# Kernel tuning notes

Measured on AMD Instinct MI355X. Metric: run time of the kernel, lower is better.

Reference implementation:

```python
import jax, jax.numpy as jnp
import jax.lax as lax
import numpy as np

# ---- Parallel3DGeometry constants ----
B, C = 1, 1
D, H, W = 64, 96, 96          # internal volume layout (z, y, x)
V, U, A = 64, 96, 90          # detector rows, detector cols, projection angles
SX = SY = SD = 1.0            # voxel size (x, y, z)
SU = SV = 1.0                 # detector spacing
NSTEPS = H + W + 2            # upper bound on voxels crossed by an XY ray
DIAG = float(np.sqrt(SX * SX + SY * SY))
EPS = 1e-12


def _t_for(p0, dp, pmin, pmax):
    # slab entry/exit parameters, matching torch _t_for (incl. parallel-ray cases)
    par = jnp.abs(dp) < EPS
    safe = jnp.where(par, 1.0, dp)
    t0 = (pmin - p0) / safe
    t1 = (pmax - p0) / safe
    lo = jnp.minimum(t0, t1)
    hi = jnp.maximum(t0, t1)
    inside = (p0 >= pmin) & (p0 <= pmax)
    lo = jnp.where(par, jnp.where(inside, -jnp.inf, jnp.inf), lo)
    hi = jnp.where(par, jnp.where(inside, jnp.inf, -jnp.inf), hi)
    return lo, hi


def _trace():
    """Vectorized Siddon XY traversal for all A*U rays.

    Returns Is, Js (int32 [A,U,NSTEPS]) voxel indices and Ws (f32 [A,U,NSTEPS])
    segment lengths (0 where the ray has exited / padded steps).
    """
    angles = jnp.linspace(0.0, np.pi, A, endpoint=False).astype(jnp.float32)
    cos_t = jnp.cos(angles)
    sin_t = jnp.sin(angles)
    u = (jnp.arange(U, dtype=jnp.float32) - (U - 1) / 2.0) * SU
    dx = jnp.broadcast_to(cos_t[:, None], (A, U)).reshape(-1)
    dy = jnp.broadcast_to(sin_t[:, None], (A, U)).reshape(-1)
    x0 = (-u[None, :] * sin_t[:, None]).reshape(-1)
    y0 = (u[None, :] * cos_t[:, None]).reshape(-1)

    x_min = -((W - 1) / 2.0) * SX; x_max = ((W - 1) / 2.0) * SX
    y_min = -((H - 1) / 2.0) * SY; y_max = ((H - 1) / 2.0) * SY
    tx0, tx1 = _t_for(x0, dx, x_min, x_max)
    ty0, ty1 = _t_for(y0, dy, y_min, y_max)
    t_entry = jnp.maximum(tx0, ty0)
    t_exit = jnp.minimum(tx1, ty1)
    alive0 = t_entry < t_exit
    te = jnp.where(alive0, t_entry, 0.0)
    tex = jnp.where(alive0, t_exit, 0.0)
    xe = x0 + te * dx
    ye = y0 + te * dy
    i0 = jnp.clip(jnp.round(xe / SX + (W - 1) / 2.0), 0, W - 1).astype(jnp.int32)
    j0 = jnp.clip(jnp.round(ye / SY + (H - 1) / 2.0), 0, H - 1).astype(jnp.int32)
    cxw = (W - 1) / 2.0 * SX
    cyh = (H - 1) / 2.0 * SY

    def body(st, _):
        i, j, x, y, t, alive = st
        valid = alive & (t < tex - EPS)
        fi = i.astype(jnp.float32)
        fj = j.astype(jnp.float32)
        xn = jnp.where(dx > 0, (fi + 0.5) * SX - cxw,
                       jnp.where(dx < 0, (fi - 0.5) * SX - cxw, jnp.inf))
        yn = jnp.where(dy > 0, (fj + 0.5) * SY - cyh,
                       jnp.where(dy < 0, (fj - 0.5) * SY - cyh, jnp.inf))
        okx = jnp.abs(dx) > EPS
        oky = jnp.abs(dy) > EPS
        tx = jnp.where(okx, (xn - x) / jnp.where(okx, dx, 1.0), jnp.inf)
        ty = jnp.where(oky, (yn - y) / jnp.where(oky, dy, 1.0), jnp.inf)
        dt = jnp.minimum(jnp.minimum(tx, ty), tex - t)
        seg = jnp.maximum(0.0, dt * DIAG / jnp.maximum(jnp.abs(dx) + jnp.abs(dy), EPS))
        w = jnp.where(valid, seg, 0.0)
        i_n = i + jnp.where(tx <= ty, jnp.where(dx > 0, 1, -1), 0)
        j_n = j + jnp.where(ty <= tx, jnp.where(dy > 0, 1, -1), 0)
        inb = (i_n >= 0) & (i_n < W) & (j_n >= 0) & (j_n < H)
        dts = jnp.where(valid, dt, 0.0)
        st2 = (jnp.where(valid, i_n, i), jnp.where(valid, j_n, j),
               x + dx * dts, y + dy * dts, t + dts, valid & inb)
        return st2, (i, j, w)

    init = (i0, j0, xe, ye, te, alive0)
    _, (Is, Js, Ws) = lax.scan(body, init, None, length=NSTEPS)
    # [NSTEPS, R] -> [A, U, NSTEPS]
    Is = Is.T.reshape(A, U, NSTEPS)
    Js = Js.T.reshape(A, U, NSTEPS)
    Ws = Ws.T.reshape(A, U, NSTEPS)
    return Is, Js, Ws


def _forward(vol):
    # model-facing [B,C,X,Y,Z] -> internal [B,C,D,H,W]
    vol_int = jnp.transpose(vol, (0, 1, 4, 3, 2))
    Is, Js, Ws = _trace()
    v_phys = (jnp.arange(V, dtype=jnp.float32) - (V - 1) / 2.0) * SV
    k = jnp.clip(jnp.round(v_phys / SD + (D - 1) / 2.0), 0, D - 1).astype(jnp.int32)
    # gather voxel values along every ray: [B,C,V,A,U,NSTEPS]
    g = vol_int[:, :, k[:, None, None, None], Js[None], Is[None]]
    out = jnp.einsum('bcvaun,aun->bcvau', g, Ws.astype(vol.dtype))
    # internal [B,C,V,A,U] (== out[b,c,a,v,u] reordered) -> model-facing [B,C,U,A,V]
    return jnp.transpose(out, (0, 1, 4, 3, 2))


def setup_inputs() -> dict:
    key = jax.random.key(0)
    vol = jax.random.normal(key, (B, C, W, H, D), dtype=jnp.float32)
    return {"vol": vol}


def reference(vol):
    return _forward(vol)
```

## Files before the change

### kernel.cpp

```cpp
#include <hip/hip_runtime.h>
#include <math.h>

namespace {
constexpr int NA = 90, NU = 96, NV = 64, NW = 96, NH = 96, ND = 64;
constexpr int NRAY  = NA * NU;
constexpr int NENT  = 256;
constexpr int CNTMAX = 208;
constexpr int TILE  = 8;
constexpr int NBLK  = NRAY / TILE;
}

__global__ __launch_bounds__(512)
void siddon_fused(const float* __restrict__ vol, float* __restrict__ out)
{
    __shared__ int2 sEnt[TILE][NENT];
    __shared__ int  sCnt[TILE];

    const int tid  = threadIdx.x;
    const int wid  = tid >> 6;
    const int lane = tid & 63;
    const int tile = blockIdx.x;
    const int ray  = tile * TILE + wid;
    const int a    = ray / NU;
    const int u    = ray - a * NU;

    const float EPSf = 1e-12f;
    const float INFp = __builtin_inff();
    const float DIAG = 1.41421356237309514547f;

    const float ang = (float)a * (float)(3.14159265358979323846 / 90.0);
    const float dx = (float)cos((double)ang);
    const float dy = (float)sin((double)ang);
    const float uu = (float)u - 47.5f;
    const float x0 = __fmul_rn(-uu, dy);
    const float y0 = __fmul_rn( uu, dx);

    const float xmin = -47.5f, xmax = 47.5f;
    const float ymin = -47.5f, ymax = 47.5f;

    float tx0, tx1;
    {
        const bool par = fabsf(dx) < EPSf;
        const float safe = par ? 1.0f : dx;
        const float t0 = __fdiv_rn(xmin - x0, safe);
        const float t1 = __fdiv_rn(xmax - x0, safe);
        const float lo = fminf(t0, t1), hi = fmaxf(t0, t1);
        const bool inside = (x0 >= xmin) && (x0 <= xmax);
        tx0 = par ? (inside ? -INFp : INFp) : lo;
        tx1 = par ? (inside ?  INFp : -INFp) : hi;
    }
    float ty0, ty1;
    {
        const bool par = fabsf(dy) < EPSf;
        const float safe = par ? 1.0f : dy;
        const float t0 = __fdiv_rn(ymin - y0, safe);
        const float t1 = __fdiv_rn(ymax - y0, safe);
        const float lo = fminf(t0, t1), hi = fmaxf(t0, t1);
        const bool inside = (y0 >= ymin) && (y0 <= ymax);
        ty0 = par ? (inside ? -INFp : INFp) : lo;
        ty1 = par ? (inside ?  INFp : -INFp) : hi;
    }

    const float t_entry = fmaxf(tx0, ty0);
    const float t_exit  = fminf(tx1, ty1);
    const bool  alive0  = t_entry < t_exit;
    const float te  = alive0 ? t_entry : 0.0f;
    const float tex = alive0 ? t_exit  : 0.0f;

    const float xe = __fadd_rn(x0, __fmul_rn(te, dx));
    const float ye = __fadd_rn(y0, __fmul_rn(te, dy));
    const int i0 = (int)fminf(fmaxf(rintf(__fadd_rn(xe, 47.5f)), 0.0f), 95.0f);
    const int j0 = (int)fminf(fmaxf(rintf(__fadd_rn(ye, 47.5f)), 0.0f), 95.0f);

    const bool okx = fabsf(dx) > EPSf;
    const bool oky = fabsf(dy) > EPSf;
    const float inv_dx = okx ? __fdiv_rn(1.0f, dx) : 0.0f;
    const float inv_dy = oky ? __fdiv_rn(1.0f, dy) : 0.0f;
    const float wscale = __fdiv_rn(DIAG, fmaxf(fabsf(dx) + fabsf(dy), EPSf));
    const float tex_m_eps = __fadd_rn(tex, -EPSf);

    const float cx = (dx > 0.0f) ? -47.0f : -48.0f;
    const float cy = (dy > 0.0f) ? -47.0f : -48.0f;
    const float Ax = okx ? __fadd_rn(te, __fmul_rn(((float)i0 + cx) - xe, inv_dx)) : INFp;
    const float Ay = oky ? __fadd_rn(te, __fmul_rn(((float)j0 + cy) - ye, inv_dy)) : INFp;
    const float px = okx ? fabsf(inv_dx) : 0.0f;
    const float py = oky ? fabsf(inv_dy) : 0.0f;
    const int   si = (dx > 0.0f) ? 1 : -1;
    const int   sj = (dy > 0.0f) ? 1 : -1;

    const float inv_pq = __fdiv_rn(1.0f, px + py);
    const float Cc = Ay - Ax;

    int2* __restrict__ myRow = &sEnt[wid][0];
    int cnt = 0;
    #pragma unroll
    for (int rnd = 0; rnd < 4; ++rnd) {
        const int n = (rnd << 6) + lane;
        const float nf = (float)n;

        float kf = __fmul_rn(__fmaf_rn(nf, py, Cc), inv_pq);
        kf = fminf(fmaxf(kf, 0.0f), nf);
        int k = (int)rintf(kf);

        #pragma unroll
        for (int it = 0; it < 4; ++it) {
            const int m = n - k;
            const float Txk   = __fmaf_rn((float)k, px, Ax);
            const float Txkm1 = (k > 0) ? __fmaf_rn((float)(k - 1), px, Ax) : -INFp;
            const float Tyl   = __fmaf_rn((float)m, py, Ay);
            const float Tylm1 = (m > 0) ? __fmaf_rn((float)(m - 1), py, Ay) : -INFp;
            const bool dec = (Txkm1 > Tyl);
            const bool inc = (!dec) && (Tylm1 > Txk);
            k += inc ? 1 : (dec ? -1 : 0);
        }

        const int m = n - k;
        const float Txk   = __fmaf_rn((float)k, px, Ax);
        const float Txkm1 = (k > 0) ? __fmaf_rn((float)(k - 1), px, Ax) : -INFp;
        const float Tyl   = __fmaf_rn((float)m, py, Ay);
        const float Tylm1 = (m > 0) ? __fmaf_rn((float)(m - 1), py, Ay) : -INFp;

        const float Tn   = fminf(Txk, Tyl);
        const float prev = fmaxf(te, fmaxf(Txkm1, Tylm1));
        const float dt   = __fadd_rn(fminf(Tn, tex), -fminf(prev, tex));
        const bool active = alive0 && (prev < tex_m_eps);
        float w = __fmul_rn(fmaxf(0.0f, dt), wscale);
        w = active ? w : 0.0f;

        const int ii = min(95, max(0, i0 + ((si > 0) ? k : -k)));
        const int jj = min(95, max(0, j0 + ((sj > 0) ? m : -m)));
        int2 e;
        e.x = (ii * NH + jj) << 8;
        e.y = __float_as_int(w);
        myRow[n] = e;

        cnt += (int)__popcll(__ballot(active));
    }
    if (lane == 0) sCnt[wid] = min((cnt + 15) & ~15, CNTMAX);
    __syncthreads();

    const int r   = lane >> 4;
    const int sub = lane & 15;
    const int subOff = sub << 4;

    const int cap = sCnt[wid];
    const int2* __restrict__ eRow = &sEnt[wid][r];
    const char* __restrict__ vb   = (const char*)vol;

    float4 aA = {0,0,0,0}, aB = {0,0,0,0}, aC = {0,0,0,0}, aD = {0,0,0,0};
    for (int n = 0; n < cap; n += 16) {
        const int2 e0 = eRow[n];
        const int2 e1 = eRow[n + 4];
        const int2 e2 = eRow[n + 8];
        const int2 e3 = eRow[n + 12];
        const float w0 = __int_as_float(e0.y);
        const float w1 = __int_as_float(e1.y);
        const float w2 = __int_as_float(e2.y);
        const float w3 = __int_as_float(e3.y);
        const float4 v0 = *(const float4*)(vb + (e0.x + subOff));
        const float4 v1 = *(const float4*)(vb + (e1.x + subOff));
        const float4 v2 = *(const float4*)(vb + (e2.x + subOff));
        const float4 v3 = *(const float4*)(vb + (e3.x + subOff));
        aA.x = fmaf(w0, v0.x, aA.x); aA.y = fmaf(w0, v0.y, aA.y);
        aA.z = fmaf(w0, v0.z, aA.z); aA.w = fmaf(w0, v0.w, aA.w);
        aB.x = fmaf(w1, v1.x, aB.x); aB.y = fmaf(w1, v1.y, aB.y);
        aB.z = fmaf(w1, v1.z, aB.z); aB.w = fmaf(w1, v1.w, aB.w);
        aC.x = fmaf(w2, v2.x, aC.x); aC.y = fmaf(w2, v2.y, aC.y);
        aC.z = fmaf(w2, v2.z, aC.z); aC.w = fmaf(w2, v2.w, aC.w);
        aD.x = fmaf(w3, v3.x, aD.x); aD.y = fmaf(w3, v3.y, aD.y);
        aD.z = fmaf(w3, v3.z, aD.z); aD.w = fmaf(w3, v3.w, aD.w);
    }
    float sx = (aA.x + aB.x) + (aC.x + aD.x);
    float sy = (aA.y + aB.y) + (aC.y + aD.y);
    float sz = (aA.z + aB.z) + (aC.z + aD.z);
    float sw = (aA.w + aB.w) + (aC.w + aD.w);

    sx += __shfl_xor(sx, 16, 64);  sy += __shfl_xor(sy, 16, 64);
    sz += __shfl_xor(sz, 16, 64);  sw += __shfl_xor(sw, 16, 64);
    sx += __shfl_xor(sx, 32, 64);  sy += __shfl_xor(sy, 32, 64);
    sz += __shfl_xor(sz, 32, 64);  sw += __shfl_xor(sw, 32, 64);

    if (lane < 16) {
        float4 res; res.x = sx; res.y = sy; res.z = sz; res.w = sw;
        *(float4*)(out + (u * NA + a) * NV + (sub << 2)) = res;
    }
}

extern "C" void kernel_launch(void* const* d_in, const int* in_sizes, int n_in,
                              void* d_out, int out_size, void* d_ws, size_t ws_size,
                              hipStream_t stream) {
    const float* vol = (const float*)d_in[0];
    float* out = (float*)d_out;
    hipLaunchKernelGGL(siddon_fused, dim3(NBLK), dim3(512), 0, stream, vol, out);
}
```

Before: 70.41 us.

## Prefetch volume into cache, inline sincos polynomial, drop block barrier

Each block now issues early float4 loads over a distinct 1/(NBLK/8) slice of the volume so the whole volume gets pulled into cache while ray setup runs; an empty asm keeps those loads live. The library double cos/sin calls are replaced with an inline double-precision polynomial sincos over the [0, pi) range. The per-wave count is kept in a register, which removes the shared sCnt array and the __syncthreads. Together these aim to cut cold-miss latency in the gather loop, math-library overhead and barrier stalls, at the cost of extra registers and redundant memory traffic.

```diff
diff --git a/kernel.cpp b/kernel.cpp
--- a/kernel.cpp
+++ b/kernel.cpp
@@ -3,18 +3,46 @@
 
 namespace {
 constexpr int NA = 90, NU = 96, NV = 64, NW = 96, NH = 96, ND = 64;
-constexpr int NRAY  = NA * NU;
-constexpr int NENT  = 256;
+constexpr int NRAY   = NA * NU;
+constexpr int NVOX   = NW * NH * ND;
+constexpr int NENT   = 256;
 constexpr int CNTMAX = 208;
-constexpr int TILE  = 8;
-constexpr int NBLK  = NRAY / TILE;
+constexpr int TILE   = 8;
+constexpr int NBLK   = NRAY / TILE;
+}
+
+__device__ inline void sincos_poly(double xd, float* s, float* c)
+{
+    const double INV_PIO2 = 0.63661977236758134308;
+    const double PIO2_HI  = 1.57079632679489655800e+00;
+    const double PIO2_LO  = 6.12323399573676603587e-17;
+    const double qd = rint(xd * INV_PIO2);
+    const double r  = (xd - qd * PIO2_HI) - qd * PIO2_LO;
+    const double z  = r * r;
+    const double sp = r + (r * z) * (-1.66666666666666324348e-01 + z *
+                     ( 8.33333333332248946124e-03 + z *
+                     (-1.98412698298579493134e-04 + z *
+                     ( 2.75573137070700676789e-06 + z *
+                     (-2.50507602534068634195e-08 + z *
+                       1.58969099521155010221e-10)))));
+    const double cp = 1.0 + z * (-0.5 + z *
+                     ( 4.16666666666666019037e-02 + z *
+                     (-1.38888888888741095749e-03 + z *
+                     ( 2.48015872894767294178e-05 + z *
+                     (-2.75573143513906633035e-07 + z *
+                     ( 2.08757232129817482790e-09 + z *
+                      -1.13596475577881948265e-11))))));
+    const int q = (int)qd;
+    const double sv = (q == 0) ? sp : ((q == 1) ? cp : -sp);
+    const double cv = (q == 0) ? cp : ((q == 1) ? -sp : -cp);
+    *s = (float)sv;
+    *c = (float)cv;
 }
 
 __global__ __launch_bounds__(512)
 void siddon_fused(const float* __restrict__ vol, float* __restrict__ out)
 {
     __shared__ int2 sEnt[TILE][NENT];
-    __shared__ int  sCnt[TILE];
 
     const int tid  = threadIdx.x;
     const int wid  = tid >> 6;
@@ -24,13 +52,24 @@
     const int a    = ray / NU;
     const int u    = ray - a * NU;
 
+    float4 wA = {0, 0, 0, 0}, wB = {0, 0, 0, 0};
+    {
+        const int nchunks = NVOX / 4;
+        const int base = (tile >> 3) * 1093;
+        const int iA = base + tid;
+        const int iB = base + 512 + tid;
+        const int hi = min(base + 1093, nchunks);
+        if (iA < hi) wA = *(const float4*)(vol + (size_t)iA * 4);
+        if (iB < hi) wB = *(const float4*)(vol + (size_t)iB * 4);
+    }
+
     const float EPSf = 1e-12f;
     const float INFp = __builtin_inff();
     const float DIAG = 1.41421356237309514547f;
 
     const float ang = (float)a * (float)(3.14159265358979323846 / 90.0);
-    const float dx = (float)cos((double)ang);
-    const float dy = (float)sin((double)ang);
+    float dy, dx;
+    sincos_poly((double)ang, &dy, &dx);
     const float uu = (float)u - 47.5f;
     const float x0 = __fmul_rn(-uu, dy);
     const float y0 = __fmul_rn( uu, dx);
@@ -136,44 +175,46 @@
 
         cnt += (int)__popcll(__ballot(active));
     }
-    if (lane == 0) sCnt[wid] = min((cnt + 15) & ~15, CNTMAX);
-    __syncthreads();
+    const int cap = min((cnt + 15) & ~15, CNTMAX);
+
+    asm volatile("" :: "v"(wA.x), "v"(wA.y), "v"(wA.z), "v"(wA.w),
+                       "v"(wB.x), "v"(wB.y), "v"(wB.z), "v"(wB.w));
 
     const int r   = lane >> 4;
     const int sub = lane & 15;
     const int subOff = sub << 4;
 
-    const int cap = sCnt[wid];
     const int2* __restrict__ eRow = &sEnt[wid][r];
     const char* __restrict__ vb   = (const char*)vol;
 
-    float4 aA = {0,0,0,0}, aB = {0,0,0,0}, aC = {0,0,0,0}, aD = {0,0,0,0};
+    float4 acc[4] = {{0,0,0,0}, {0,0,0,0}, {0,0,0,0}, {0,0,0,0}};
     for (int n = 0; n < cap; n += 16) {
         const int2 e0 = eRow[n];
         const int2 e1 = eRow[n + 4];
         const int2 e2 = eRow[n + 8];
         const int2 e3 = eRow[n + 12];
+        const float4 v0 = *(const float4*)(vb + (e0.x + subOff));
+        const float4 v1 = *(const float4*)(vb + (e1.x + subOff));
+        const float4 v2 = *(const float4*)(vb + (e2.x + subOff));
+        const float4 v3 = *(const float4*)(vb + (e3.x + subOff));
         const float w0 = __int_as_float(e0.y);
         const float w1 = __int_as_float(e1.y);
         const float w2 = __int_as_float(e2.y);
         const float w3 = __int_as_float(e3.y);
-        const float4 v0 = *(const float4*)(vb + (e0.x + subOff));
-        const float4 v1 = *(const float4*)(vb + (e1.x + subOff));
-        const float4 v2 = *(const float4*)(vb + (e2.x + subOff));
-        const float4 v3 = *(const float4*)(vb + (e3.x + subOff));
-        aA.x = fmaf(w0, v0.x, aA.x); aA.y = fmaf(w0, v0.y, aA.y);
-        aA.z = fmaf(w0, v0.z, aA.z); aA.w = fmaf(w0, v0.w, aA.w);
-        aB.x = fmaf(w1, v1.x, aB.x); aB.y = fmaf(w1, v1.y, aB.y);
-        aB.z = fmaf(w1, v1.z, aB.z); aB.w = fmaf(w1, v1.w, aB.w);
-        aC.x = fmaf(w2, v2.x, aC.x); aC.y = fmaf(w2, v2.y, aC.y);
-        aC.z = fmaf(w2, v2.z, aC.z); aC.w = fmaf(w2, v2.w, aC.w);
-        aD.x = fmaf(w3, v3.x, aD.x); aD.y = fmaf(w3, v3.y, aD.y);
-        aD.z = fmaf(w3, v3.z, aD.z); aD.w = fmaf(w3, v3.w, aD.w);
-    }
-    float sx = (aA.x + aB.x) + (aC.x + aD.x);
-    float sy = (aA.y + aB.y) + (aC.y + aD.y);
-    float sz = (aA.z + aB.z) + (aC.z + aD.z);
-    float sw = (aA.w + aB.w) + (aC.w + aD.w);
+        acc[0].x = fmaf(w0, v0.x, acc[0].x); acc[0].y = fmaf(w0, v0.y, acc[0].y);
+        acc[0].z = fmaf(w0, v0.z, acc[0].z); acc[0].w = fmaf(w0, v0.w, acc[0].w);
+        acc[1].x = fmaf(w1, v1.x, acc[1].x); acc[1].y = fmaf(w1, v1.y, acc[1].y);
+        acc[1].z = fmaf(w1, v1.z, acc[1].z); acc[1].w = fmaf(w1, v1.w, acc[1].w);
+        acc[2].x = fmaf(w2, v2.x, acc[2].x); acc[2].y = fmaf(w2, v2.y, acc[2].y);
+        acc[2].z = fmaf(w2, v2.z, acc[2].z); acc[2].w = fmaf(w2, v2.w, acc[2].w);
+        acc[3].x = fmaf(w3, v3.x, acc[3].x); acc[3].y = fmaf(w3, v3.y, acc[3].y);
+        acc[3].z = fmaf(w3, v3.z, acc[3].z); acc[3].w = fmaf(w3, v3.w, acc[3].w);
+    }
+
+    float sx = (acc[0].x + acc[1].x) + (acc[2].x + acc[3].x);
+    float sy = (acc[0].y + acc[1].y) + (acc[2].y + acc[3].y);
+    float sz = (acc[0].z + acc[1].z) + (acc[2].z + acc[3].z);
+    float sw = (acc[0].w + acc[1].w) + (acc[2].w + acc[3].w);
 
     sx += __shfl_xor(sx, 16, 64);  sy += __shfl_xor(sy, 16, 64);
     sz += __shfl_xor(sz, 16, 64);  sw += __shfl_xor(sw, 16, 64);
```

After: 67.92 us. 3.5% less time.
